# Kernel tuning notes

Measured on AMD Instinct MI355X. Metric: run time of the kernel, lower is better.

## Reference

```python
import jax, jax.numpy as jnp
import numpy as np

K = 9                 # num_keypoints
NA = 1                # num_anchors
NC = 1                # num_classes
NB, NH, NW = 16, 76, 76
NUM_LABELS = 2 * K + 3
MAX_T = 50
COORD_SCALE = 1.0
OBJECT_SCALE = 5.0
NOOBJECT_SCALE = 0.1
SIL_THRESH = 0.6
DIST_THRESH = 30.0
IM_W, IM_H = 640.0, 480.0
PRETRAIN_EPOCHS = 15
SHARP = 2.0           # sharpness in corner_confidences


def corner_conf(gt, pr):
    """gt, pr: [..., K, 2] normalized corner coords -> mean per-keypoint confidence [...]."""
    scale = jnp.asarray([IM_W, IM_H], dtype=gt.dtype)
    d = (gt - pr) * scale
    dist = jnp.sqrt(jnp.sum(d * d, axis=-1))                       # [..., K] pixel distance
    c = (jnp.exp(SHARP * (1.0 - dist / DIST_THRESH)) - 1.0) / (np.exp(SHARP) - 1.0)
    c = jnp.where(dist < DIST_THRESH, c, 0.0)
    return jnp.mean(c, axis=-1)


def setup_inputs() -> dict:
    key = jax.random.key(0)
    k1, k2 = jax.random.split(key)
    output = jax.random.normal(k1, (NB, NA * (2 * K + 1 + NC), NH, NW), dtype=jnp.float32)
    target = jax.random.uniform(k2, (NB, MAX_T * NUM_LABELS), dtype=jnp.float32)
    return {"output": output, "target": target, "epoch": 20}


def reference(output, target, epoch):
    out = output.reshape(NB, NA, 2 * K + 1 + NC, NH, NW)
    xs = out[:, :, 0:2 * K:2]                                      # [NB,NA,K,NH,NW]
    ys = out[:, :, 1:2 * K:2]
    xs = jnp.concatenate([jax.nn.sigmoid(xs[:, :, :1]), xs[:, :, 1:]], axis=2)  # sigmoid only kp0
    ys = jnp.concatenate([jax.nn.sigmoid(ys[:, :, :1]), ys[:, :, 1:]], axis=2)
    conf = jax.nn.sigmoid(out[:, :, 2 * K])                        # [NB,NA,NH,NW]

    # ---- predicted corners (detached, as in torch: x[i].data) ----
    xd = jax.lax.stop_gradient(xs)
    yd = jax.lax.stop_gradient(ys)
    grid_x = jnp.arange(NW, dtype=jnp.float32)
    grid_y = jnp.arange(NH, dtype=jnp.float32)
    px = (xd + grid_x[None, None, None, None, :]) / NW
    py = (yd + grid_y[None, None, None, :, None]) / NH
    pred = jnp.stack([px, py], axis=-1)                            # [NB,NA,K,NH,NW,2]
    pred = pred.transpose(0, 1, 3, 4, 2, 5).reshape(NB, NA * NH * NW, K, 2)

    # ---- ground-truth parsing ----
    tgt = jax.lax.stop_gradient(target).reshape(NB, MAX_T, NUM_LABELS)
    gt = tgt[:, :, 1:1 + 2 * K].reshape(NB, MAX_T, K, 2)           # normalized corners
    # loop breaks at first t with target[...,1]==0 -> prefix validity
    valid = jnp.cumprod((tgt[:, :, 1] != 0).astype(jnp.int32), axis=1).astype(bool)  # [NB,MAX_T]

    # ---- phase 1: silent-threshold conf mask ----
    confs = corner_conf(gt[:, :, None], pred[:, None])             # [NB,MAX_T,nAnchors]
    confs = jnp.where(valid[:, :, None], confs, 0.0)
    cur_confs = jnp.max(confs, axis=1)                             # running max, init 0 (confs>=0)
    conf_mask = jnp.where(cur_confs > SIL_THRESH, 0.0, NOOBJECT_SCALE).reshape(NB, NA, NH, NW)

    # ---- phase 2: per-GT assignment (best_n = 0) ----
    gx_all = gt[..., 0] * NW                                       # [NB,MAX_T,K]
    gy_all = gt[..., 1] * NH
    gi0 = gx_all[:, :, 0].astype(jnp.int32)                        # centroid cell
    gj0 = gy_all[:, :, 0].astype(jnp.int32)
    b_idx = jnp.broadcast_to(jnp.arange(NB)[:, None], (NB, MAX_T))
    gi = jnp.where(valid, gi0, NW)                                 # OOB index -> dropped scatter
    gj = jnp.where(valid, gj0, NH)
    a0 = jnp.zeros_like(gi)

    coord_mask = jnp.zeros((NB, NA, NH, NW)).at[b_idx, a0, gj, gi].set(1.0, mode='drop')
    conf_mask = conf_mask.at[b_idx, a0, gj, gi].set(OBJECT_SCALE, mode='drop')

    tx_vals = gx_all - gi0[..., None].astype(jnp.float32)          # [NB,MAX_T,K]
    ty_vals = gy_all - gj0[..., None].astype(jnp.float32)
    txs = jnp.zeros((NB, NA, NH, NW, K)).at[b_idx, a0, gj, gi].set(tx_vals, mode='drop')
    tys = jnp.zeros((NB, NA, NH, NW, K)).at[b_idx, a0, gj, gi].set(ty_vals, mode='drop')

    cell = jnp.clip(gj0 * NW + gi0, 0, NH * NW - 1)                # anchor-0 cell index
    pred_cells = pred.reshape(NB, NA, NH * NW, K, 2)[b_idx, 0, cell]  # [NB,MAX_T,K,2]
    tconf_vals = corner_conf(gt, pred_cells)                       # [NB,MAX_T]
    tconf = jnp.zeros((NB, NA, NH, NW)).at[b_idx, a0, gj, gi].set(tconf_vals, mode='drop')

    # ---- losses ----
    m = coord_mask[:, :, None]                                     # broadcast over K
    txs_t = jnp.moveaxis(txs, -1, 2)                               # [NB,NA,K,NH,NW]
    tys_t = jnp.moveaxis(tys, -1, 2)
    loss_x = COORD_SCALE * 0.5 * jnp.sum((xs * m - txs_t * m) ** 2)
    loss_y = COORD_SCALE * 0.5 * jnp.sum((ys * m - tys_t * m) ** 2)
    cm = jnp.sqrt(conf_mask)
    loss_conf = 0.5 * jnp.sum((conf * cm - tconf * cm) ** 2)
    if epoch > PRETRAIN_EPOCHS:
        loss = loss_x + loss_y + loss_conf
    else:
        loss = loss_x + loss_y
    return loss
```

## Files before the change

### kernel.cpp

```cpp
#include <hip/hip_runtime.h>
#include <math.h>

#define KPT 9
#define NB 16
#define NH 76
#define NW 76
#define MAX_T 50
#define NCH 20
#define NUM_LABELS 21
#define CELLS (NH*NW)
#define IM_W 640.0f
#define IM_H 480.0f
#define SX (IM_W/(float)NW)
#define SY (IM_H/(float)NH)
#define DIST_THRESH 30.0f
#define D2_THRESH (DIST_THRESH*DIST_THRESH)
#define SIL_THRESH 0.6f
#define OBJECT_SCALE 5.0f
#define NOOBJECT_SCALE 0.1f
#define PRETRAIN_EPOCHS 15
#define E2M1 6.3890560989306495f
#define CNORM (1.0f/(E2M1*9.0f))
#define CURMAX_BREAK (SIL_THRESH * E2M1 * 9.0f)
#define CNT_MIN 6

#define TSPLIT 8
#define CPB 64
#define NTHREADS (TSPLIT*64)

__device__ __forceinline__ float sigmoidf_(float x) {
    return 1.0f / (1.0f + __expf(-x));
}

__global__ void zero_out_kernel(float* d_out) {
    d_out[0] = 0.0f;
}

__launch_bounds__(NTHREADS)
__global__ void region_loss_kernel(const float* __restrict__ output,
                                   const float* __restrict__ target,
                                   const int* __restrict__ epoch_p,
                                   float* __restrict__ d_out)
{
    const int tid  = threadIdx.x;
    const int wave = tid >> 6;
    const int cl   = tid & 63;
    const int b    = blockIdx.y;
    const int cell = blockIdx.x * CPB + cl;
    const bool live = (cell < CELLS);

    __shared__ float4 s_gt4[MAX_T][5];
    __shared__ float2 s_txy[MAX_T][KPT];
    __shared__ float  s_tconf[MAX_T];
    __shared__ int    s_nvalid;
    __shared__ int    s_win[CPB];
    __shared__ float  s_sil[TSPLIT][CPB];

    const float* tgb = target + (size_t)b * MAX_T * NUM_LABELS;

    if (tid < 64) {
        float v1 = (tid < MAX_T) ? tgb[tid * NUM_LABELS + 1] : 1.0f;
        unsigned long long zm = __ballot(v1 == 0.0f);
        if (tid == 0) {
            int fz = (zm == 0ULL) ? MAX_T : (__ffsll((long long)zm) - 1);
            s_nvalid = fz < MAX_T ? fz : MAX_T;
        }
        s_win[tid] = -1;
    }
    __syncthreads();

    if (tid < MAX_T) {
        const float* row = tgb + tid * NUM_LABELS;
        float gx0 = row[1] * (float)NW;
        float gy0 = row[2] * (float)NH;
        int gi0 = (int)gx0;
        int gj0 = (int)gy0;
        int cellt = gj0 * NW + gi0;
        int cellc = min(max(cellt, 0), CELLS - 1);
        int hc = cellc / NW, wc = cellc % NW;
        const float* ob = output + (size_t)b * NCH * CELLS + cellc;
        float* gdst = (float*)&s_gt4[tid][0];
        float csum = 0.0f;
        #pragma unroll
        for (int k = 0; k < KPT; ++k) {
            float gxk = row[1 + 2*k];
            float gyk = row[2 + 2*k];
            float gxp = gxk * IM_W;
            float gyp = gyk * IM_H;
            gdst[2*k]   = gxp;
            gdst[2*k+1] = gyp;
            s_txy[tid][k] = make_float2(gxk * (float)NW - (float)gi0,
                                        gyk * (float)NH - (float)gj0);
            float xo = ob[(2*k) * CELLS];
            float yo = ob[(2*k + 1) * CELLS];
            if (k == 0) { xo = sigmoidf_(xo); yo = sigmoidf_(yo); }
            float dx = gxp - (xo + (float)wc) * SX;
            float dy = gyp - (yo + (float)hc) * SY;
            float d2 = dx*dx + dy*dy;
            if (d2 < D2_THRESH) {
                csum += __expf(2.0f - sqrtf(d2) * (2.0f / DIST_THRESH)) - 1.0f;
            }
        }
        gdst[18] = 1e18f; gdst[19] = 1e18f;
        s_tconf[tid] = csum * CNORM;
        bool scatter_ok = (gi0 >= 0 && gi0 < NW && gj0 >= 0 && gj0 < NH) &&
                          (tid < s_nvalid);
        int c = cellt - blockIdx.x * CPB;
        if (scatter_ok && c >= 0 && c < CPB) atomicMax(&s_win[c], tid);
    }
    __syncthreads();

    const int nv = s_nvalid;

    float pxs[KPT], pys[KPT];
    float sil = 0.0f;
    if (live) {
        const int h = cell / NW;
        const int w = cell - h * NW;
        const float* ob = output + (size_t)b * NCH * CELLS + cell;
        #pragma unroll
        for (int k = 0; k < KPT; ++k) {
            float xo = ob[(2*k) * CELLS];
            float yo = ob[(2*k + 1) * CELLS];
            if (k == 0) { xo = sigmoidf_(xo); yo = sigmoidf_(yo); }
            pxs[k] = (xo + (float)w) * SX;
            pys[k] = (yo + (float)h) * SY;
        }
        for (int t = wave; t < nv; t += TSPLIT) {
            float4 q0 = s_gt4[t][0];
            float4 q1 = s_gt4[t][1];
            float4 q2 = s_gt4[t][2];
            float4 q3 = s_gt4[t][3];
            float4 q4 = s_gt4[t][4];
            int cnt = 0;
            #define KP(gx, gy, k) { \
                float dx = (gx) - pxs[k]; \
                float dy = (gy) - pys[k]; \
                float d2 = __builtin_fmaf(dx, dx, dy*dy); \
                cnt += (d2 < D2_THRESH) ? 1 : 0; }
            KP(q0.x, q0.y, 0) KP(q0.z, q0.w, 1)
            KP(q1.x, q1.y, 2) KP(q1.z, q1.w, 3)
            KP(q2.x, q2.y, 4) KP(q2.z, q2.w, 5)
            KP(q3.x, q3.y, 6) KP(q3.z, q3.w, 7)
            KP(q4.x, q4.y, 8)
            #undef KP
            if (cnt >= CNT_MIN) {
                const float* gq = (const float*)&s_gt4[t][0];
                float csum = 0.0f;
                #pragma unroll
                for (int k = 0; k < KPT; ++k) {
                    float dx = gq[2*k]   - pxs[k];
                    float dy = gq[2*k+1] - pys[k];
                    float d2 = __builtin_fmaf(dx, dx, dy*dy);
                    if (d2 < D2_THRESH)
                        csum += __expf(2.0f - sqrtf(d2) * (2.0f / DIST_THRESH)) - 1.0f;
                }
                if (csum > CURMAX_BREAK) sil = 1.0f;
            }
        }
    }
    s_sil[wave][cl] = sil;
    __syncthreads();

    float contrib = 0.0f;
    if (wave == 0 && live) {
        float sl = 0.0f;
        #pragma unroll
        for (int wv = 0; wv < TSPLIT; ++wv) sl = fmaxf(sl, s_sil[wv][cl]);
        const int wn = s_win[cl];
        const int h = cell / NW;
        const int w = cell - h * NW;
        const float* ob = output + (size_t)b * NCH * CELLS + cell;
        const float conf = sigmoidf_(ob[2*KPT * CELLS]);

        float cmask, tconf;
        if (wn >= 0) {
            cmask = OBJECT_SCALE;
            tconf = s_tconf[wn];
            #pragma unroll
            for (int k = 0; k < KPT; ++k) {
                float xo = pxs[k] * (1.0f/SX) - (float)w;
                float yo = pys[k] * (1.0f/SY) - (float)h;
                float2 txy = s_txy[wn][k];
                float dxv = xo - txy.x;
                float dyv = yo - txy.y;
                contrib += 0.5f * (dxv*dxv + dyv*dyv);
            }
        } else {
            cmask = (sl > 0.0f) ? 0.0f : NOOBJECT_SCALE;
            tconf = 0.0f;
        }
        if (epoch_p[0] > PRETRAIN_EPOCHS) {
            float d = conf - tconf;
            contrib += 0.5f * cmask * d * d;
        }
    }

    if (wave == 0) {
        #pragma unroll
        for (int off = 32; off > 0; off >>= 1)
            contrib += __shfl_down(contrib, off);
        if (cl == 0) atomicAdd(d_out, contrib);
    }
}

extern "C" void kernel_launch(void* const* d_in, const int* in_sizes, int n_in,
                              void* d_out, int out_size, void* d_ws, size_t ws_size,
                              hipStream_t stream) {
    const float* output = (const float*)d_in[0];
    const float* target = (const float*)d_in[1];
    const int*   epoch  = (const int*)d_in[2];
    float* out = (float*)d_out;

    zero_out_kernel<<<1, 1, 0, stream>>>(out);

    dim3 grid((CELLS + CPB - 1) / CPB, NB);
    region_loss_kernel<<<grid, NTHREADS, 0, stream>>>(output, target, epoch, out);
}
```

Measured before the change: 35.51 us.

## Hoist per-batch target parsing into a precompute kernel shared via workspace

Moves the per-batch ground-truth parsing, tconf computation and winner-cell assignment out of every block into a separate 16-block precompute kernel that writes records and a per-cell winner map to workspace. The zeroing kernel is folded into it. The main kernel reads GT records from global memory with software prefetch of the next record instead of building them in shared memory per block. This removes redundant per-block target work and two __syncthreads. In exchange it adds a tiny serial kernel, a full winner-map write of NB*CELLS ints, and global/L2 reads in the inner loop.

Result: slower. 37.22 us (+4.8%).

```diff
diff --git a/kernel.cpp b/kernel.cpp
--- a/kernel.cpp
+++ b/kernel.cpp
@@ -28,46 +28,32 @@
 #define CPB 64
 #define NTHREADS (TSPLIT*64)
 
+#define TREC 40
+#define GT_FLOATS (NB*MAX_T*TREC)
+
 __device__ __forceinline__ float sigmoidf_(float x) {
     return 1.0f / (1.0f + __expf(-x));
 }
 
-__global__ void zero_out_kernel(float* d_out) {
-    d_out[0] = 0.0f;
-}
-
-__launch_bounds__(NTHREADS)
-__global__ void region_loss_kernel(const float* __restrict__ output,
-                                   const float* __restrict__ target,
-                                   const int* __restrict__ epoch_p,
-                                   float* __restrict__ d_out)
+__global__ void precompute_kernel(const float* __restrict__ output,
+                                  const float* __restrict__ target,
+                                  float* __restrict__ wsf,
+                                  int* __restrict__ W,
+                                  int* __restrict__ nvA,
+                                  float* __restrict__ d_out)
 {
-    const int tid  = threadIdx.x;
-    const int wave = tid >> 6;
-    const int cl   = tid & 63;
-    const int b    = blockIdx.y;
-    const int cell = blockIdx.x * CPB + cl;
-    const bool live = (cell < CELLS);
-
-    __shared__ float4 s_gt4[MAX_T][5];
-    __shared__ float2 s_txy[MAX_T][KPT];
-    __shared__ float  s_tconf[MAX_T];
-    __shared__ int    s_nvalid;
-    __shared__ int    s_win[CPB];
-    __shared__ float  s_sil[TSPLIT][CPB];
-
+    const int b   = blockIdx.x;
+    const int tid = threadIdx.x;
     const float* tgb = target + (size_t)b * MAX_T * NUM_LABELS;
 
-    if (tid < 64) {
-        float v1 = (tid < MAX_T) ? tgb[tid * NUM_LABELS + 1] : 1.0f;
-        unsigned long long zm = __ballot(v1 == 0.0f);
-        if (tid == 0) {
-            int fz = (zm == 0ULL) ? MAX_T : (__ffsll((long long)zm) - 1);
-            s_nvalid = fz < MAX_T ? fz : MAX_T;
-        }
-        s_win[tid] = -1;
-    }
-    __syncthreads();
+    float v1 = (tid < MAX_T) ? tgb[tid * NUM_LABELS + 1] : 1.0f;
+    unsigned long long zm = __ballot(v1 == 0.0f);
+    int nv = (zm == 0ULL) ? MAX_T : (__ffsll((long long)zm) - 1);
+    if (nv > MAX_T) nv = MAX_T;
+
+    for (int i = tid; i < CELLS; i += 64) W[(size_t)b * CELLS + i] = -1;
+
+    __shared__ int s_cellA[MAX_T];
 
     if (tid < MAX_T) {
         const float* row = tgb + tid * NUM_LABELS;
@@ -79,7 +65,7 @@
         int cellc = min(max(cellt, 0), CELLS - 1);
         int hc = cellc / NW, wc = cellc % NW;
         const float* ob = output + (size_t)b * NCH * CELLS + cellc;
-        float* gdst = (float*)&s_gt4[tid][0];
+        float* rec = wsf + ((size_t)b * MAX_T + tid) * TREC;
         float csum = 0.0f;
         #pragma unroll
         for (int k = 0; k < KPT; ++k) {
@@ -87,30 +73,54 @@
             float gyk = row[2 + 2*k];
             float gxp = gxk * IM_W;
             float gyp = gyk * IM_H;
-            gdst[2*k]   = gxp;
-            gdst[2*k+1] = gyp;
-            s_txy[tid][k] = make_float2(gxk * (float)NW - (float)gi0,
-                                        gyk * (float)NH - (float)gj0);
+            rec[2*k]      = gxp;
+            rec[2*k + 1]  = gyp;
+            rec[20 + 2*k] = gxk * (float)NW - (float)gi0;
+            rec[21 + 2*k] = gyk * (float)NH - (float)gj0;
             float xo = ob[(2*k) * CELLS];
             float yo = ob[(2*k + 1) * CELLS];
             if (k == 0) { xo = sigmoidf_(xo); yo = sigmoidf_(yo); }
             float dx = gxp - (xo + (float)wc) * SX;
             float dy = gyp - (yo + (float)hc) * SY;
             float d2 = dx*dx + dy*dy;
-            if (d2 < D2_THRESH) {
+            if (d2 < D2_THRESH)
                 csum += __expf(2.0f - sqrtf(d2) * (2.0f / DIST_THRESH)) - 1.0f;
-            }
-        }
-        gdst[18] = 1e18f; gdst[19] = 1e18f;
-        s_tconf[tid] = csum * CNORM;
-        bool scatter_ok = (gi0 >= 0 && gi0 < NW && gj0 >= 0 && gj0 < NH) &&
-                          (tid < s_nvalid);
-        int c = cellt - blockIdx.x * CPB;
-        if (scatter_ok && c >= 0 && c < CPB) atomicMax(&s_win[c], tid);
+        }
+        rec[18] = 1e18f; rec[19] = 1e18f;
+        rec[38] = csum * CNORM;
+        rec[39] = 0.0f;
+        bool ok = (gi0 >= 0 && gi0 < NW && gj0 >= 0 && gj0 < NH) && (tid < nv);
+        s_cellA[tid] = ok ? cellt : -1;
     }
     __syncthreads();
-
-    const int nv = s_nvalid;
+    if (tid == 0) {
+        for (int t = 0; t < nv; ++t) {
+            int c = s_cellA[t];
+            if (c >= 0) W[(size_t)b * CELLS + c] = t;
+        }
+        nvA[b] = nv;
+        if (b == 0) d_out[0] = 0.0f;
+    }
+}
+
+__launch_bounds__(NTHREADS)
+__global__ void region_loss_kernel(const float* __restrict__ output,
+                                   const float* __restrict__ wsf,
+                                   const int* __restrict__ W,
+                                   const int* __restrict__ nvA,
+                                   const int* __restrict__ epoch_p,
+                                   float* __restrict__ d_out)
+{
+    const int tid  = threadIdx.x;
+    const int wave = tid >> 6;
+    const int cl   = tid & 63;
+    const int b    = blockIdx.y;
+    const int cell = blockIdx.x * CPB + cl;
+    const bool live = (cell < CELLS);
+
+    __shared__ float s_sil[TSPLIT][CPB];
+
+    const int nv = nvA[b];
 
     float pxs[KPT], pys[KPT];
     float sil = 0.0f;
@@ -126,37 +136,50 @@
             pxs[k] = (xo + (float)w) * SX;
             pys[k] = (yo + (float)h) * SY;
         }
-        for (int t = wave; t < nv; t += TSPLIT) {
-            float4 q0 = s_gt4[t][0];
-            float4 q1 = s_gt4[t][1];
-            float4 q2 = s_gt4[t][2];
-            float4 q3 = s_gt4[t][3];
-            float4 q4 = s_gt4[t][4];
+
+        const float* base = wsf + (size_t)b * MAX_T * TREC;
+        float4 c0 = {0,0,0,0}, c1 = c0, c2 = c0, c3 = c0, c4 = c0;
+        float4 n0 = c0, n1 = c0, n2 = c0, n3 = c0, n4 = c0;
+        int t = wave;
+        if (t < nv) {
+            const float4* g = (const float4*)(base + t * TREC);
+            c0 = g[0]; c1 = g[1]; c2 = g[2]; c3 = g[3]; c4 = g[4];
+        }
+        for (; t < nv; t += TSPLIT) {
+            const int tn = t + TSPLIT;
+            if (tn < nv) {
+                const float4* g = (const float4*)(base + tn * TREC);
+                n0 = g[0]; n1 = g[1]; n2 = g[2]; n3 = g[3]; n4 = g[4];
+            }
             int cnt = 0;
             #define KP(gx, gy, k) { \
                 float dx = (gx) - pxs[k]; \
                 float dy = (gy) - pys[k]; \
                 float d2 = __builtin_fmaf(dx, dx, dy*dy); \
                 cnt += (d2 < D2_THRESH) ? 1 : 0; }
-            KP(q0.x, q0.y, 0) KP(q0.z, q0.w, 1)
-            KP(q1.x, q1.y, 2) KP(q1.z, q1.w, 3)
-            KP(q2.x, q2.y, 4) KP(q2.z, q2.w, 5)
-            KP(q3.x, q3.y, 6) KP(q3.z, q3.w, 7)
-            KP(q4.x, q4.y, 8)
+            KP(c0.x, c0.y, 0) KP(c0.z, c0.w, 1)
+            KP(c1.x, c1.y, 2) KP(c1.z, c1.w, 3)
+            KP(c2.x, c2.y, 4) KP(c2.z, c2.w, 5)
+            KP(c3.x, c3.y, 6) KP(c3.z, c3.w, 7)
+            KP(c4.x, c4.y, 8)
             #undef KP
             if (cnt >= CNT_MIN) {
-                const float* gq = (const float*)&s_gt4[t][0];
                 float csum = 0.0f;
-                #pragma unroll
-                for (int k = 0; k < KPT; ++k) {
-                    float dx = gq[2*k]   - pxs[k];
-                    float dy = gq[2*k+1] - pys[k];
-                    float d2 = __builtin_fmaf(dx, dx, dy*dy);
-                    if (d2 < D2_THRESH)
-                        csum += __expf(2.0f - sqrtf(d2) * (2.0f / DIST_THRESH)) - 1.0f;
-                }
+                #define KQ(gx, gy, k) { \
+                    float dx = (gx) - pxs[k]; \
+                    float dy = (gy) - pys[k]; \
+                    float d2 = __builtin_fmaf(dx, dx, dy*dy); \
+                    if (d2 < D2_THRESH) \
+                        csum += __expf(2.0f - sqrtf(d2) * (2.0f / DIST_THRESH)) - 1.0f; }
+                KQ(c0.x, c0.y, 0) KQ(c0.z, c0.w, 1)
+                KQ(c1.x, c1.y, 2) KQ(c1.z, c1.w, 3)
+                KQ(c2.x, c2.y, 4) KQ(c2.z, c2.w, 5)
+                KQ(c3.x, c3.y, 6) KQ(c3.z, c3.w, 7)
+                KQ(c4.x, c4.y, 8)
+                #undef KQ
                 if (csum > CURMAX_BREAK) sil = 1.0f;
             }
+            c0 = n0; c1 = n1; c2 = n2; c3 = n3; c4 = n4;
         }
     }
     s_sil[wave][cl] = sil;
@@ -167,7 +190,7 @@
         float sl = 0.0f;
         #pragma unroll
         for (int wv = 0; wv < TSPLIT; ++wv) sl = fmaxf(sl, s_sil[wv][cl]);
-        const int wn = s_win[cl];
+        const int wn = W[(size_t)b * CELLS + cell];
         const int h = cell / NW;
         const int w = cell - h * NW;
         const float* ob = output + (size_t)b * NCH * CELLS + cell;
@@ -175,15 +198,15 @@
 
         float cmask, tconf;
         if (wn >= 0) {
+            const float* rec = wsf + ((size_t)b * MAX_T + wn) * TREC;
             cmask = OBJECT_SCALE;
-            tconf = s_tconf[wn];
+            tconf = rec[38];
             #pragma unroll
             for (int k = 0; k < KPT; ++k) {
                 float xo = pxs[k] * (1.0f/SX) - (float)w;
                 float yo = pys[k] * (1.0f/SY) - (float)h;
-                float2 txy = s_txy[wn][k];
-                float dxv = xo - txy.x;
-                float dyv = yo - txy.y;
+                float dxv = xo - rec[20 + 2*k];
+                float dyv = yo - rec[21 + 2*k];
                 contrib += 0.5f * (dxv*dxv + dyv*dyv);
             }
         } else {
@@ -212,8 +235,12 @@
     const int*   epoch  = (const int*)d_in[2];
     float* out = (float*)d_out;
 
-    zero_out_kernel<<<1, 1, 0, stream>>>(out);
+    float* wsf = (float*)d_ws;
+    int*   W   = (int*)(wsf + GT_FLOATS);
+    int*   nvA = W + (size_t)NB * CELLS;
+
+    precompute_kernel<<<NB, 64, 0, stream>>>(output, target, wsf, W, nvA, out);
 
     dim3 grid((CELLS + CPB - 1) / CPB, NB);
-    region_loss_kernel<<<grid, NTHREADS, 0, stream>>>(output, target, epoch, out);
-}
+    region_loss_kernel<<<grid, NTHREADS, 0, stream>>>(output, wsf, W, nvA, epoch, out);
+}
```
